# Optimization experiments

Hardware: AMD Instinct MI355X
Metric: run time of the kernel (lower is better)

The kernel has to match this reference:

```python
import jax, jax.numpy as jnp
import numpy as np

N, D_IN, D_OUT, E, TOPK = 2048, 2048, 2048, 8, 2


def setup_inputs() -> dict:
    key = jax.random.key(0)
    k1, k2, k3, k4 = jax.random.split(key, 4)
    inputs = jax.random.normal(k1, (N, D_IN), dtype=jnp.float32)
    weight = jax.random.normal(k2, (E, D_OUT, D_IN), dtype=jnp.float32) * (1.0 / np.sqrt(D_IN))
    gates = jax.random.uniform(k3, (N, TOPK), dtype=jnp.float32)
    gates = gates / jnp.sum(gates, axis=-1, keepdims=True)
    # random routing: expert id for each of the N*TOPK (token, slot) pairs
    expert_of = jax.random.randint(k4, (N * TOPK,), 0, E, dtype=jnp.int32)
    order = jnp.argsort(expert_of)  # positions sorted by expert id
    sorted_expert_idxs = expert_of[order].astype(jnp.int32)
    sorted_scattered_idxs = order.astype(jnp.int32)
    counts = jnp.bincount(expert_of, length=E)
    expert_offsets = jnp.cumsum(counts).astype(jnp.int32)
    padded_block_idxs = jnp.zeros((1,), dtype=jnp.int32)  # kernel blocking artifact, no math effect
    return {
        "inputs": inputs,
        "weight": weight,
        "k": TOPK,
        "sorted_expert_idxs": sorted_expert_idxs,
        "sorted_scattered_idxs": sorted_scattered_idxs,
        "padded_block_idxs": padded_block_idxs,
        "expert_offsets": expert_offsets,
        "gates": gates,
    }


def reference(inputs, weight, k, sorted_expert_idxs, sorted_scattered_idxs,
              padded_block_idxs, expert_offsets, gates):
    # inputs: [N, d_in]; weight: [E, d_out, d_in] (module permutes to [E, d_in, d_out])
    n_tok, d_in = inputs.shape
    n_e, d_out, _ = weight.shape
    nk = sorted_expert_idxs.shape[0]
    # invert the sort: expert id per flat (token, slot) position
    expert_of = jnp.zeros((nk,), dtype=sorted_expert_idxs.dtype).at[sorted_scattered_idxs].set(sorted_expert_idxs)
    x_flat = inputs[jnp.arange(nk) // k]  # [N*k, d_in] (fan-out of k per token)
    # grouped GEMM: y_flat[j] = x_flat[j] @ weight[expert_of[j]].T
    y_flat = jnp.zeros((nk, d_out), dtype=inputs.dtype)
    for e in range(n_e):  # loop over fixed small expert count (structural)
        mask = (expert_of == e)[:, None]
        y_flat = y_flat + jnp.where(mask, x_flat, 0.0) @ weight[e].T
    # gating combine: bmm(gates[:, None, :], y.view(N, k, d_out))
    out = jnp.einsum('nk,nkd->nd', gates, y_flat.reshape(n_tok, k, d_out))
    return out
```

## Files before the change

### kernel.cpp

```cpp
#include <hip/hip_runtime.h>
#include <hip/hip_bf16.h>

#define DIN   2048
#define DOUT  2048
#define NTOK  2048
#define NE    8
#define TOPK  2
#define NK    (NTOK*TOPK)
#define BM    128
#define BN    128
#define BK    64
#define NKT   (DIN/BK)
#define MAXMT (NK/BM + NE)
#define NTN   (DOUT/BN)
#define NBLK  (MAXMT*NTN)

#define WEL (NE*DOUT*DIN)
#define XEL (NTOK*DIN)

typedef unsigned short u16;
typedef __attribute__((ext_vector_type(8))) short bf16x8;
typedef __attribute__((ext_vector_type(4))) float f32x4;

__device__ __forceinline__ unsigned pack2rn(float a, float b) {
    union { float f; unsigned u; } x, y; x.f = a; y.f = b;
    return __builtin_amdgcn_perm(y.u + 0x8000u, x.u + 0x8000u, 0x07060302u);
}

__device__ __forceinline__ void gl_lds16(const void* g, void* l) {
    __builtin_amdgcn_global_load_lds(
        (const __attribute__((address_space(1))) void*)g,
        (__attribute__((address_space(3)))       void*)l, 16, 0, 0);
}

__global__ __launch_bounds__(256) void cvt_bf16(
    const float* __restrict__ w, const float* __restrict__ x,
    u16* __restrict__ wbf, u16* __restrict__ xbf)
{
    const size_t nch = (size_t)(WEL + XEL) / 8;
    for (size_t c = (size_t)blockIdx.x * blockDim.x + threadIdx.x; c < nch;
         c += (size_t)gridDim.x * blockDim.x) {
        const float* src; u16* dst; size_t off;
        if (c < (size_t)WEL / 8) { src = w; dst = wbf; off = c * 8; }
        else                     { src = x; dst = xbf; off = (c - (size_t)WEL / 8) * 8; }
        float4 f0 = *(const float4*)(src + off);
        float4 f1 = *(const float4*)(src + off + 4);
        uint4 pk;
        pk.x = pack2rn(f0.x, f0.y); pk.y = pack2rn(f0.z, f0.w);
        pk.z = pack2rn(f1.x, f1.y); pk.w = pack2rn(f1.z, f1.w);
        *(uint4*)(dst + off) = pk;
    }
}

__global__ __launch_bounds__(512, 4) void moe_gemm_tlp(
    const u16* __restrict__ xb,
    const u16* __restrict__ wb,
    const int* __restrict__ sorted_scattered_idxs,
    const int* __restrict__ expert_offsets,
    const float* __restrict__ gates,
    float*     __restrict__ out)
{
    __shared__ u16 As[2][BM * BK];
    __shared__ u16 Bs[2][BN * BK];
    __shared__ int   s_tok[BM];
    __shared__ float s_gate[BM];

    const int bid = blockIdx.x;
    const int swz = (bid & 7) * (NBLK / 8) + (bid >> 3);
    const int n0  = (swz & (NTN - 1)) * BN;
    const int mt  = swz >> 4;

    int e = -1, m0 = 0, cnt = 0;
    {
        int acc0 = 0, prev = 0;
        for (int i = 0; i < NE; ++i) {
            int end = expert_offsets[i];
            int c = end - prev;
            int t = (c + BM - 1) / BM;
            if (mt < acc0 + t) {
                e = i; m0 = prev + (mt - acc0) * BM;
                cnt = end - m0; if (cnt > BM) cnt = BM;
                break;
            }
            acc0 += t; prev = end;
        }
    }
    if (e < 0) return;

    const int tid = threadIdx.x;
    if (tid < BM) {
        int idx = (tid < cnt) ? (m0 + tid) : m0;
        int p = sorted_scattered_idxs[idx];
        s_tok[tid]  = p;
        s_gate[tid] = gates[p];
    }
    __syncthreads();

    const int wid = tid >> 6, lane = tid & 63;

    const u16* wbE = wb + (size_t)e * DOUT * DIN;
    const int ch   = tid & 7;
    const int row0 = tid >> 3;
    const int cg   = ch ^ (row0 & 7);
    const u16* aS[2]; const u16* bS[2];
    #pragma unroll
    for (int s = 0; s < 2; ++s) {
        int r = row0 + s * 64;
        aS[s] = xb  + (size_t)(s_tok[r] >> 1) * DIN + cg * 8;
        bS[s] = wbE + (size_t)(n0 + r) * DIN + cg * 8;
    }
    const int dst0 = wid * 512;
    const int dst1 = wid * 512 + 4096;

    const int wr = wid >> 2, wc = wid & 3;
    const int lr = lane & 15, g = lane >> 4;
    const int xk0 = ((0 + g) ^ (lr & 7)) * 8;
    const int xk1 = ((4 + g) ^ (lr & 7)) * 8;
    int aoff[4], boff[2];
    #pragma unroll
    for (int mi = 0; mi < 4; ++mi) aoff[mi] = (wr * 64 + mi * 16 + lr) * BK;
    #pragma unroll
    for (int n = 0; n < 2; ++n)    boff[n]  = (wc * 32 + n * 16 + lr) * BK;

    f32x4 acc[4][2];
    #pragma unroll
    for (int mi = 0; mi < 4; ++mi)
        #pragma unroll
        for (int n = 0; n < 2; ++n) acc[mi][n] = (f32x4)0.0f;

#define STG(buf, t)                                                           \
    {                                                                         \
        const int ko = (t) * BK;                                              \
        gl_lds16(aS[0] + ko, &As[buf][dst0]);                                 \
        gl_lds16(aS[1] + ko, &As[buf][dst1]);                                 \
        gl_lds16(bS[0] + ko, &Bs[buf][dst0]);                                 \
        gl_lds16(bS[1] + ko, &Bs[buf][dst1]);                                 \
    }

#define BODY(t)                                                               \
    {                                                                         \
        const int b = (t) & 1;                                                \
        bf16x8 af[4][2], bf[2][2];                                            \
        _Pragma("unroll")                                                     \
        for (int mi = 0; mi < 4; ++mi) {                                      \
            af[mi][0] = *(const bf16x8*)(&As[b][aoff[mi] + xk0]);             \
            af[mi][1] = *(const bf16x8*)(&As[b][aoff[mi] + xk1]);             \
        }                                                                     \
        _Pragma("unroll")                                                     \
        for (int n = 0; n < 2; ++n) {                                         \
            bf[n][0] = *(const bf16x8*)(&Bs[b][boff[n] + xk0]);               \
            bf[n][1] = *(const bf16x8*)(&Bs[b][boff[n] + xk1]);               \
        }                                                                     \
        asm volatile("s_waitcnt lgkmcnt(0)" ::: "memory");                    \
        __builtin_amdgcn_sched_barrier(0);                                    \
        __builtin_amdgcn_s_setprio(1);                                        \
        _Pragma("unroll")                                                     \
        for (int mi = 0; mi < 4; ++mi)                                        \
            _Pragma("unroll")                                                 \
            for (int n = 0; n < 2; ++n) {                                     \
                acc[mi][n] = __builtin_amdgcn_mfma_f32_16x16x32_bf16(         \
                    af[mi][0], bf[n][0], acc[mi][n], 0, 0, 0);                \
                acc[mi][n] = __builtin_amdgcn_mfma_f32_16x16x32_bf16(         \
                    af[mi][1], bf[n][1], acc[mi][n], 0, 0, 0);                \
            }                                                                 \
        __builtin_amdgcn_s_setprio(0);                                        \
        __builtin_amdgcn_s_barrier();                                         \
    }

    STG(0, 0);
    STG(1, 1);

    for (int t = 0; t < NKT - 2; ++t) {
        asm volatile("s_waitcnt vmcnt(4)" ::: "memory");
        __builtin_amdgcn_sched_barrier(0);
        __builtin_amdgcn_s_barrier();
        BODY(t);
        STG(t & 1, t + 2);
    }
    {
        asm volatile("s_waitcnt vmcnt(4)" ::: "memory");
        __builtin_amdgcn_sched_barrier(0);
        __builtin_amdgcn_s_barrier();
        BODY(NKT - 2);
    }
    {
        asm volatile("s_waitcnt vmcnt(0)" ::: "memory");
        __builtin_amdgcn_sched_barrier(0);
        __builtin_amdgcn_s_barrier();
        BODY(NKT - 1);
    }

#undef STG
#undef BODY

    #pragma unroll
    for (int mi = 0; mi < 4; ++mi) {
        #pragma unroll
        for (int r = 0; r < 4; ++r) {
            int lrow = wr * 64 + mi * 16 + g * 4 + r;
            if (lrow < cnt) {
                int   p  = s_tok[lrow];
                float gf = s_gate[lrow];
                float* orow = out + (size_t)(p >> 1) * DOUT + n0 + wc * 32;
                #pragma unroll
                for (int n = 0; n < 2; ++n)
                    atomicAdd(orow + n * 16 + lr, gf * acc[mi][n][r]);
            }
        }
    }
}

#define FBM 128
#define FBK 64
__global__ __launch_bounds__(256, 3) void moe_gemm_fused(
    const float* __restrict__ inputs, const float* __restrict__ weight,
    const int* __restrict__ sorted_scattered_idxs, const int* __restrict__ expert_offsets,
    const float* __restrict__ gates, float* __restrict__ out)
{
    __shared__ u16 As[FBM * FBK];
    __shared__ u16 Bs[FBM * FBK];
    __shared__ int   s_tok[FBM];
    __shared__ float s_gate[FBM];

    const int mt = blockIdx.y;
    const int n0 = blockIdx.x * FBM;
    int e = -1, m0 = 0, cnt = 0;
    {
        int acc = 0, prev = 0;
        for (int i = 0; i < NE; ++i) {
            int end = expert_offsets[i];
            int c = end - prev;
            int t = (c + FBM - 1) / FBM;
            if (mt < acc + t) {
                e = i; m0 = prev + (mt - acc) * FBM;
                cnt = end - m0; if (cnt > FBM) cnt = FBM;
                break;
            }
            acc += t; prev = end;
        }
    }
    if (e < 0) return;

    const int tid = threadIdx.x;
    if (tid < FBM) {
        int idx = (tid < cnt) ? (m0 + tid) : m0;
        int p = sorted_scattered_idxs[idx];
        s_tok[tid]  = p;
        s_gate[tid] = gates[p];
    }
    __syncthreads();

    const int ch  = tid & 7;
    const int r0  = tid >> 3;
    const int sch = ch ^ (r0 & 7);
    const float* wbase = weight + (size_t)e * DOUT * DIN;
    const float* ap[4]; const float* bp[4];
    #pragma unroll
    for (int i = 0; i < 4; ++i) {
        int r = r0 + 32 * i;
        ap[i] = inputs + (size_t)(s_tok[r] >> 1) * DIN + ch * 8;
        bp[i] = wbase + (size_t)(n0 + r) * DIN + ch * 8;
    }
    u16* aw = &As[r0 * FBK + sch * 8];
    u16* bw = &Bs[r0 * FBK + sch * 8];

    const int wid = tid >> 6, lane = tid & 63;
    const int wm = (wid >> 1) * 64, wn = (wid & 1) * 64;
    const int g  = lane >> 4, lr = lane & 15;

    f32x4 acc[4][4];
    #pragma unroll
    for (int i = 0; i < 4; ++i)
        #pragma unroll
        for (int j = 0; j < 4; ++j) acc[i][j] = (f32x4)0.0f;

    float4 pa[4][2], pb[4][2];
    #pragma unroll
    for (int i = 0; i < 4; ++i) {
        pa[i][0] = *(const float4*)(ap[i] + 0); pa[i][1] = *(const float4*)(ap[i] + 4);
        pb[i][0] = *(const float4*)(bp[i] + 0); pb[i][1] = *(const float4*)(bp[i] + 4);
    }
    for (int kt = 0; kt < DIN / FBK; ++kt) {
        __syncthreads();
        #pragma unroll
        for (int i = 0; i < 4; ++i) {
            uint4 va, vb;
            va.x = pack2rn(pa[i][0].x, pa[i][0].y); va.y = pack2rn(pa[i][0].z, pa[i][0].w);
            va.z = pack2rn(pa[i][1].x, pa[i][1].y); va.w = pack2rn(pa[i][1].z, pa[i][1].w);
            *(uint4*)(aw + i * 32 * FBK) = va;
            vb.x = pack2rn(pb[i][0].x, pb[i][0].y); vb.y = pack2rn(pb[i][0].z, pb[i][0].w);
            vb.z = pack2rn(pb[i][1].x, pb[i][1].y); vb.w = pack2rn(pb[i][1].z, pb[i][1].w);
            *(uint4*)(bw + i * 32 * FBK) = vb;
        }
        __syncthreads();
        if (kt + 1 < DIN / FBK) {
            const int kof = (kt + 1) * FBK;
            #pragma unroll
            for (int i = 0; i < 4; ++i) {
                pa[i][0] = *(const float4*)(ap[i] + kof); pa[i][1] = *(const float4*)(ap[i] + kof + 4);
                pb[i][0] = *(const float4*)(bp[i] + kof); pb[i][1] = *(const float4*)(bp[i] + kof + 4);
            }
        }
        #pragma unroll
        for (int ks = 0; ks < 2; ++ks) {
            bf16x8 a[4], b[4];
            #pragma unroll
            for (int i = 0; i < 4; ++i) {
                int ra = wm + i * 16 + lr; int ca = (ks * 4 + g) ^ (ra & 7);
                a[i] = *(const bf16x8*)(&As[ra * FBK + ca * 8]);
                int rb = wn + i * 16 + lr; int cb = (ks * 4 + g) ^ (rb & 7);
                b[i] = *(const bf16x8*)(&Bs[rb * FBK + cb * 8]);
            }
            #pragma unroll
            for (int i = 0; i < 4; ++i)
                #pragma unroll
                for (int j = 0; j < 4; ++j)
                    acc[i][j] = __builtin_amdgcn_mfma_f32_16x16x32_bf16(a[i], b[j], acc[i][j], 0, 0, 0);
        }
    }
    #pragma unroll
    for (int i = 0; i < 4; ++i) {
        #pragma unroll
        for (int j2 = 0; j2 < 4; ++j2) {
            int lrow = wm + i * 16 + g * 4 + j2;
            if (lrow < cnt) {
                int   p  = s_tok[lrow];
                float gf = s_gate[lrow];
                float* orow = out + (size_t)(p >> 1) * DOUT + n0 + wn;
                #pragma unroll
                for (int nf = 0; nf < 4; ++nf)
                    atomicAdd(orow + nf * 16 + lr, gf * acc[i][nf][j2]);
            }
        }
    }
}

extern "C" void kernel_launch(void* const* d_in, const int* in_sizes, int n_in,
                              void* d_out, int out_size, void* d_ws, size_t ws_size,
                              hipStream_t stream) {
    const float* inputs  = (const float*)d_in[0];
    const float* weight  = (const float*)d_in[1];
    const int*   ssi     = (const int*)d_in[4];
    const int*   eoff    = (const int*)d_in[6];
    const float* gates   = (const float*)d_in[7];
    float* out = (float*)d_out;

    hipMemsetAsync(out, 0, (size_t)out_size * sizeof(float), stream);

    const size_t need = ((size_t)WEL + (size_t)XEL) * sizeof(u16);
    if (ws_size >= need) {
        u16* wbf = (u16*)d_ws;
        u16* xbf = wbf + (size_t)WEL;
        cvt_bf16<<<2048, 256, 0, stream>>>(weight, inputs, wbf, xbf);
        moe_gemm_tlp<<<NBLK, 512, 0, stream>>>(xbf, wbf, ssi, eoff, gates, out);
    } else {
        dim3 grid(DOUT / FBM, NK / FBM + NE);
        moe_gemm_fused<<<grid, 256, 0, stream>>>(inputs, weight, ssi, eoff, gates, out);
    }
}
```

Baseline: 113.2 us.

## Fuse fp32-to-bf16 weight conversion into GEMM B-tile loading

Removes the separate pass that converted all expert weights to bf16 in a workspace. Only the activations are pre-converted now. The GEMM loads fp32 weight tiles into registers, packs them to bf16, and stores them to LDS with a one-stage register prefetch. This avoids writing and re-reading the whole bf16 weight copy, at the cost of double-width weight reads per tile and a less asynchronous B pipeline.

```diff
diff --git a/kernel.cpp b/kernel.cpp
--- a/kernel.cpp
+++ b/kernel.cpp
@@ -33,32 +33,29 @@
         (__attribute__((address_space(3)))       void*)l, 16, 0, 0);
 }
 
-__global__ __launch_bounds__(256) void cvt_bf16(
-    const float* __restrict__ w, const float* __restrict__ x,
-    u16* __restrict__ wbf, u16* __restrict__ xbf)
+__global__ __launch_bounds__(256) void cvt_x(
+    const float* __restrict__ x, u16* __restrict__ xbf)
 {
-    const size_t nch = (size_t)(WEL + XEL) / 8;
+    const size_t nch = (size_t)XEL / 8;
     for (size_t c = (size_t)blockIdx.x * blockDim.x + threadIdx.x; c < nch;
          c += (size_t)gridDim.x * blockDim.x) {
-        const float* src; u16* dst; size_t off;
-        if (c < (size_t)WEL / 8) { src = w; dst = wbf; off = c * 8; }
-        else                     { src = x; dst = xbf; off = (c - (size_t)WEL / 8) * 8; }
-        float4 f0 = *(const float4*)(src + off);
-        float4 f1 = *(const float4*)(src + off + 4);
+        size_t off = c * 8;
+        float4 f0 = *(const float4*)(x + off);
+        float4 f1 = *(const float4*)(x + off + 4);
         uint4 pk;
         pk.x = pack2rn(f0.x, f0.y); pk.y = pack2rn(f0.z, f0.w);
         pk.z = pack2rn(f1.x, f1.y); pk.w = pack2rn(f1.z, f1.w);
-        *(uint4*)(dst + off) = pk;
-    }
-}
-
-__global__ __launch_bounds__(512, 4) void moe_gemm_tlp(
-    const u16* __restrict__ xb,
-    const u16* __restrict__ wb,
-    const int* __restrict__ sorted_scattered_idxs,
-    const int* __restrict__ expert_offsets,
+        *(uint4*)(xbf + off) = pk;
+    }
+}
+
+__global__ __launch_bounds__(512, 4) void moe_gemm_wf(
+    const u16*   __restrict__ xb,
+    const float* __restrict__ wf,
+    const int*   __restrict__ sorted_scattered_idxs,
+    const int*   __restrict__ expert_offsets,
     const float* __restrict__ gates,
-    float*     __restrict__ out)
+    float*       __restrict__ out)
 {
     __shared__ u16 As[2][BM * BK];
     __shared__ u16 Bs[2][BN * BK];
@@ -98,19 +95,23 @@
 
     const int wid = tid >> 6, lane = tid & 63;
 
-    const u16* wbE = wb + (size_t)e * DOUT * DIN;
     const int ch   = tid & 7;
     const int row0 = tid >> 3;
     const int cg   = ch ^ (row0 & 7);
-    const u16* aS[2]; const u16* bS[2];
-    #pragma unroll
-    for (int s = 0; s < 2; ++s) {
-        int r = row0 + s * 64;
-        aS[s] = xb  + (size_t)(s_tok[r] >> 1) * DIN + cg * 8;
-        bS[s] = wbE + (size_t)(n0 + r) * DIN + cg * 8;
-    }
+    const u16* aS[2];
+    #pragma unroll
+    for (int s = 0; s < 2; ++s)
+        aS[s] = xb + (size_t)(s_tok[row0 + s * 64] >> 1) * DIN + cg * 8;
     const int dst0 = wid * 512;
     const int dst1 = wid * 512 + 4096;
+
+    const float* wbE = wf + (size_t)e * DOUT * DIN;
+    const float* bF[2];
+    #pragma unroll
+    for (int s = 0; s < 2; ++s)
+        bF[s] = wbE + (size_t)(n0 + row0 + s * 64) * DIN + ch * 8;
+    const int bwr0 = row0 * BK + cg * 8;
+    const int bwr1 = (row0 + 64) * BK + cg * 8;
 
     const int wr = wid >> 2, wc = wid & 3;
     const int lr = lane & 15, g = lane >> 4;
@@ -128,13 +129,33 @@
         #pragma unroll
         for (int n = 0; n < 2; ++n) acc[mi][n] = (f32x4)0.0f;
 
-#define STG(buf, t)                                                           \
+    float4 pb[4];
+
+#define STGA(buf, t)                                                          \
     {                                                                         \
         const int ko = (t) * BK;                                              \
         gl_lds16(aS[0] + ko, &As[buf][dst0]);                                 \
         gl_lds16(aS[1] + ko, &As[buf][dst1]);                                 \
-        gl_lds16(bS[0] + ko, &Bs[buf][dst0]);                                 \
-        gl_lds16(bS[1] + ko, &Bs[buf][dst1]);                                 \
+    }
+
+#define BGLB(t)                                                               \
+    {                                                                         \
+        const int ko = (t) * BK;                                              \
+        pb[0] = *(const float4*)(bF[0] + ko);                                 \
+        pb[1] = *(const float4*)(bF[0] + ko + 4);                             \
+        pb[2] = *(const float4*)(bF[1] + ko);                                 \
+        pb[3] = *(const float4*)(bF[1] + ko + 4);                             \
+    }
+
+#define BPACK(buf)                                                            \
+    {                                                                         \
+        uint4 w0, w1;                                                         \
+        w0.x = pack2rn(pb[0].x, pb[0].y); w0.y = pack2rn(pb[0].z, pb[0].w);   \
+        w0.z = pack2rn(pb[1].x, pb[1].y); w0.w = pack2rn(pb[1].z, pb[1].w);   \
+        w1.x = pack2rn(pb[2].x, pb[2].y); w1.y = pack2rn(pb[2].z, pb[2].w);   \
+        w1.z = pack2rn(pb[3].x, pb[3].y); w1.w = pack2rn(pb[3].z, pb[3].w);   \
+        *(uint4*)(&Bs[buf][bwr0]) = w0;                                       \
+        *(uint4*)(&Bs[buf][bwr1]) = w1;                                       \
     }
 
 #define BODY(t)                                                               \
@@ -167,30 +188,27 @@
         __builtin_amdgcn_s_barrier();                                         \
     }
 
-    STG(0, 0);
-    STG(1, 1);
-
-    for (int t = 0; t < NKT - 2; ++t) {
-        asm volatile("s_waitcnt vmcnt(4)" ::: "memory");
-        __builtin_amdgcn_sched_barrier(0);
+    BGLB(0);
+    STGA(0, 0);
+    asm volatile("s_waitcnt vmcnt(0)" ::: "memory");
+    __builtin_amdgcn_sched_barrier(0);
+    BPACK(0);
+    STGA(1, 1);
+    BGLB(1);
+
+    for (int t = 0; t < NKT; ++t) {
+        asm volatile("s_waitcnt lgkmcnt(0)" ::: "memory");
         __builtin_amdgcn_s_barrier();
         BODY(t);
-        STG(t & 1, t + 2);
-    }
-    {
-        asm volatile("s_waitcnt vmcnt(4)" ::: "memory");
-        __builtin_amdgcn_sched_barrier(0);
-        __builtin_amdgcn_s_barrier();
-        BODY(NKT - 2);
-    }
-    {
         asm volatile("s_waitcnt vmcnt(0)" ::: "memory");
         __builtin_amdgcn_sched_barrier(0);
-        __builtin_amdgcn_s_barrier();
-        BODY(NKT - 1);
-    }
-
-#undef STG
+        if (t + 1 < NKT) BPACK((t + 1) & 1);
+        if (t + 2 < NKT) { STGA(t & 1, t + 2); BGLB(t + 2); }
+    }
+
+#undef STGA
+#undef BGLB
+#undef BPACK
 #undef BODY
 
     #pragma unroll
@@ -347,12 +365,11 @@
 
     hipMemsetAsync(out, 0, (size_t)out_size * sizeof(float), stream);
 
-    const size_t need = ((size_t)WEL + (size_t)XEL) * sizeof(u16);
+    const size_t need = (size_t)XEL * sizeof(u16);
     if (ws_size >= need) {
-        u16* wbf = (u16*)d_ws;
-        u16* xbf = wbf + (size_t)WEL;
-        cvt_bf16<<<2048, 256, 0, stream>>>(weight, inputs, wbf, xbf);
-        moe_gemm_tlp<<<NBLK, 512, 0, stream>>>(xbf, wbf, ssi, eoff, gates, out);
+        u16* xbf = (u16*)d_ws;
+        cvt_x<<<1024, 256, 0, stream>>>(inputs, xbf);
+        moe_gemm_wf<<<NBLK, 512, 0, stream>>>(xbf, weight, ssi, eoff, gates, out);
     } else {
         dim3 grid(DOUT / FBM, NK / FBM + NE);
         moe_gemm_fused<<<grid, 256, 0, stream>>>(inputs, weight, ssi, eoff, gates, out);
```

Result: no change. 113.7 us (+0.5%).
